# Performance work log

Measured on AMD Instinct MI355X. Metric: run time of the kernel, lower is better.

The kernel has to match this reference:

```python
import itertools
import jax, jax.numpy as jnp
import numpy as np
from jax import lax

INT_STEPS = 7
DOWN = 2


def _sample(vol, coords):
    """Trilinear sample vol [C, D, H, W] at voxel coords [3, D2, H2, W2].
    Matches torch grid_sample(align_corners=True, padding_mode='zeros') after
    voxelmorph's voxel->[-1,1] normalization (i.e. plain voxel coordinates)."""
    dims = vol.shape[1:]
    c0f = jnp.floor(coords)
    frac = coords - c0f
    c0 = c0f.astype(jnp.int32)
    out = jnp.zeros((vol.shape[0],) + coords.shape[1:], vol.dtype)
    for corner in itertools.product((0, 1), repeat=3):
        w = jnp.ones(coords.shape[1:], vol.dtype)
        valid = True
        idxs = []
        for ax in range(3):
            idx = c0[ax] + corner[ax]
            w = w * (frac[ax] if corner[ax] else 1.0 - frac[ax])
            valid = valid & (idx >= 0) & (idx < dims[ax])
            idxs.append(jnp.clip(idx, 0, dims[ax] - 1))
        out = out + vol[:, idxs[0], idxs[1], idxs[2]] * (w * valid)
    return out


def _grid(shape, dtype):
    return jnp.stack(jnp.meshgrid(*[jnp.arange(s, dtype=dtype) for s in shape], indexing='ij'))


def _warp(src, flow):
    # SpatialTransformer: sample src at identity grid + flow (voxel coords)
    return _sample(src, _grid(src.shape[1:], flow.dtype) + flow)


def _resize(x, out_shape):
    # F.interpolate trilinear, align_corners=True: src = i*(in-1)/(out-1)
    coords = jnp.stack(jnp.meshgrid(
        *[jnp.linspace(0.0, s_in - 1.0, s_out, dtype=x.dtype)
          for s_in, s_out in zip(x.shape[1:], out_shape)], indexing='ij'))
    return _sample(x, coords)


def _flow_single(pos_flow, label):
    # pos_flow: [3, D, H, W], label: [1, D, H, W]
    full = pos_flow.shape[1:]
    down_shape = tuple(s // DOWN for s in full)
    # ResizeTransform(int_downsize): factor=1/DOWN<1 -> resize then scale
    f = _resize(pos_flow, down_shape) * (1.0 / DOWN)
    # VecInt: scaling and squaring
    f = f * (1.0 / (2 ** INT_STEPS))
    for _ in range(INT_STEPS):
        f = f + _warp(f, f)
    # ResizeTransform(1/int_downsize): factor=DOWN>1 -> scale then resize
    f = _resize(f * float(DOWN), full)
    moved = _warp(label, f)
    return moved, f


def setup_inputs() -> dict:
    key = jax.random.key(0)
    k1, k2, k3 = jax.random.split(key, 3)
    B, F, D, H, W = 1, 16, 128, 128, 128
    features = jax.random.normal(k1, (B, F, D, H, W), jnp.float32)
    moving_label = jax.random.uniform(k2, (B, 1, D, H, W), jnp.float32)
    # conv weight initialized Normal(0, 1e-5), bias zeros (as in module)
    weight = jax.random.normal(k3, (3, F, 3, 3, 3), jnp.float32) * 1e-5
    bias = jnp.zeros((3,), jnp.float32)
    return {"features": features, "moving_label": moving_label,
            "weight": weight, "bias": bias}


def reference(features, moving_label, weight, bias):
    pos_flow = lax.conv_general_dilated(
        features, weight, window_strides=(1, 1, 1),
        padding=[(1, 1)] * 3,
        dimension_numbers=('NCDHW', 'OIDHW', 'NCDHW'))
    pos_flow = pos_flow + bias[None, :, None, None, None]
    moved, flow = jax.vmap(_flow_single)(pos_flow, moving_label)
    return moved, flow
```

## Files before the change

kernel.cpp:

```cpp
#include <hip/hip_runtime.h>
#include <hip/hip_bf16.h>


#define V128 2097152
#define V64  262144

template <int C>
__device__ __forceinline__ void trisample(const float* __restrict__ vol,
                                          int D, int H, int W, int cstride,
                                          float cz, float cy, float cx,
                                          float* out) {
    float fz = floorf(cz), fy = floorf(cy), fx = floorf(cx);
    int iz = (int)fz, iy = (int)fy, ix = (int)fx;
    float tz = cz - fz, ty = cy - fy, tx = cx - fx;
#pragma unroll
    for (int c = 0; c < C; ++c) out[c] = 0.0f;
#pragma unroll
    for (int dz = 0; dz < 2; ++dz) {
#pragma unroll
        for (int dy = 0; dy < 2; ++dy) {
#pragma unroll
            for (int dx = 0; dx < 2; ++dx) {
                int z = iz + dz, y = iy + dy, x = ix + dx;
                float w = (dz ? tz : 1.0f - tz) *
                          (dy ? ty : 1.0f - ty) *
                          (dx ? tx : 1.0f - tx);
                bool valid = (z >= 0) && (z < D) && (y >= 0) && (y < H) &&
                             (x >= 0) && (x < W);
                int zc = min(max(z, 0), D - 1);
                int yc = min(max(y, 0), H - 1);
                int xc = min(max(x, 0), W - 1);
                int base = (zc * H + yc) * W + xc;
                float wv = valid ? w : 0.0f;
#pragma unroll
                for (int c = 0; c < C; ++c)
                    out[c] += vol[c * cstride + base] * wv;
            }
        }
    }
}

template <int SI>
__device__ __forceinline__ void lds_lerp3(const float* __restrict__ f,
                                          float pz, float py, float px,
                                          float* out) {
    constexpr int NI = SI * SI * SI;
    float fz = floorf(pz), fy = floorf(py), fx = floorf(px);
    int iz = (int)fz, iy = (int)fy, ix = (int)fx;
    float tz = pz - fz, ty = py - fy, tx = px - fx;
    int b = (iz * SI + iy) * SI + ix;
    float wz0 = 1.0f - tz, wy0 = 1.0f - ty, wx0 = 1.0f - tx;
#pragma unroll
    for (int c = 0; c < 3; ++c) {
        const float* fc = f + c * NI;
        float v00 = fc[b] * wx0 + fc[b + 1] * tx;
        float v01 = fc[b + SI] * wx0 + fc[b + SI + 1] * tx;
        float v10 = fc[b + SI * SI] * wx0 + fc[b + SI * SI + 1] * tx;
        float v11 = fc[b + SI * SI + SI] * wx0 + fc[b + SI * SI + SI + 1] * tx;
        out[c] = wz0 * (wy0 * v00 + ty * v01) + tz * (wy0 * v10 + ty * v11);
    }
}

template <int SI>
__device__ __forceinline__ void step_lds(const float* __restrict__ in,
                                         float* __restrict__ out, int tid) {
    constexpr int SO = SI - 2;
    constexpr int NI = SI * SI * SI;
    constexpr int NO = SO * SO * SO;
    for (int i = tid; i < NO; i += 256) {
        int xx = i % SO, yy = (i / SO) % SO, zz = i / (SO * SO);
        int la = ((zz + 1) * SI + (yy + 1)) * SI + (xx + 1);
        float fz = in[la], fy = in[la + NI], fx = in[la + 2 * NI];
        float sm[3];
        lds_lerp3<SI>(in, (zz + 1) + fz, (yy + 1) + fy, (xx + 1) + fx, sm);
        out[i] = fz + sm[0];
        out[i + NO] = fy + sm[1];
        out[i + 2 * NO] = fx + sm[2];
    }
}

__device__ __forceinline__ void step_to_global(const float* __restrict__ in,
                                               float* __restrict__ gout,
                                               int tx, int ty, int tz,
                                               int tid) {
    constexpr int SI = 10;
    constexpr int NI = SI * SI * SI;
    for (int i = tid; i < 512; i += 256) {
        int xx = i & 7, yy = (i >> 3) & 7, zz = i >> 6;
        int la = ((zz + 1) * SI + (yy + 1)) * SI + (xx + 1);
        float fz = in[la], fy = in[la + NI], fx = in[la + 2 * NI];
        float sm[3];
        lds_lerp3<SI>(in, (zz + 1) + fz, (yy + 1) + fy, (xx + 1) + fx, sm);
        int n = ((tz + zz) << 12) + ((ty + yy) << 6) + (tx + xx);
        gout[n] = fz + sm[0];
        gout[n + V64] = fy + sm[1];
        gout[n + 2 * V64] = fx + sm[2];
    }
}

__global__ __launch_bounds__(256) void conv_kernel(
    const float* __restrict__ feat, const float* __restrict__ weight,
    const float* __restrict__ bias, float* __restrict__ pos_flow) {
    __shared__ float smem[2][3960];
    const int tid = threadIdx.x;
    const int x0 = blockIdx.x * 64, y0 = blockIdx.y * 4, z0 = blockIdx.z * 8;
    const int lx = tid & 63, ly = tid >> 6;

    int goff[16];
    unsigned vmask = 0;
    {
        int xx = tid % 66;
        int r = tid / 66;
        int yy = r % 6;
        int zz = r / 6;
#pragma unroll
        for (int k = 0; k < 16; ++k) {
            bool intile = (k < 15) || (tid < 120);
            int gx = x0 + xx - 1, gy = y0 + yy - 1, gz = z0 + zz - 1;
            bool ok = intile && ((unsigned)gx < 128u) &&
                      ((unsigned)gy < 128u) && ((unsigned)gz < 128u);
            goff[k] = (gz << 14) + (gy << 7) + gx;
            if (ok) vmask |= (1u << k);
            xx += 58;
            yy += 3;
            if (xx >= 66) { xx -= 66; yy += 1; }
            if (yy >= 6) { yy -= 6; zz += 1; }
        }
    }

    typedef __attribute__((ext_vector_type(2))) float f32x2;
    f32x2 acc[3][4];
#pragma unroll
    for (int o = 0; o < 3; ++o)
#pragma unroll
        for (int zp = 0; zp < 4; ++zp) acc[o][zp] = (f32x2)(0.0f);

    {
        float vals[16];
#pragma unroll
        for (int k = 0; k < 16; ++k) {
            vals[k] = 0.0f;
            if (vmask & (1u << k)) vals[k] = feat[goff[k]];
        }
#pragma unroll
        for (int k = 0; k < 16; ++k)
            if (k < 15 || tid < 120) smem[0][tid + 256 * k] = vals[k];
    }

    for (int c = 0; c < 16; ++c) {
        __syncthreads();
        if (c + 1 < 16) {
            const float* fc = feat + ((c + 1) << 21);
            float* buf = smem[(c + 1) & 1];
            float vals[16];
#pragma unroll
            for (int k = 0; k < 16; ++k) {
                vals[k] = 0.0f;
                if (vmask & (1u << k)) vals[k] = fc[goff[k]];
            }
#pragma unroll
            for (int k = 0; k < 16; ++k)
                if (k < 15 || tid < 120) buf[tid + 256 * k] = vals[k];
        }
        const float* buf = smem[c & 1];
        const float* wc = weight + c * 27;
#pragma unroll
        for (int dy = 0; dy < 3; ++dy) {
#pragma unroll
            for (int dx = 0; dx < 3; ++dx) {
                const float* p = buf + (ly + dy) * 66 + lx + dx;
                float v[10];
#pragma unroll
                for (int zz = 0; zz < 10; ++zz) v[zz] = p[zz * 396];
#pragma unroll
                for (int dz = 0; dz < 3; ++dz) {
#pragma unroll
                    for (int o = 0; o < 3; ++o) {
                        float w = wc[o * 432 + dz * 9 + dy * 3 + dx];
#pragma unroll
                        for (int zp = 0; zp < 4; ++zp) {
                            acc[o][zp].x += v[2 * zp + dz] * w;
                            acc[o][zp].y += v[2 * zp + dz + 1] * w;
                        }
                    }
                }
            }
        }
    }

#pragma unroll
    for (int o = 0; o < 3; ++o) {
        float b = bias[o];
#pragma unroll
        for (int zp = 0; zp < 4; ++zp) {
            int z = z0 + 2 * zp;
            int base = o * V128 + ((y0 + ly) << 7) + x0 + lx;
            pos_flow[base + (z << 14)] = acc[o][zp].x + b;
            pos_flow[base + ((z + 1) << 14)] = acc[o][zp].y + b;
        }
    }
}

__global__ __launch_bounds__(256) void f2_kernel(
    const float* __restrict__ pos_flow, float* __restrict__ gout) {
    __shared__ float A[3 * 2744];
    __shared__ float B[3 * 1728];
    const int tid = threadIdx.x;
    const int tx = blockIdx.x * 8, ty = blockIdx.y * 8, tz = blockIdx.z * 8;
    const int rbx = tx - 3, rby = ty - 3, rbz = tz - 3;
    const float s2 = 127.0f / 63.0f;
    const float k = 1.0f / 256.0f;
    for (int i = tid; i < 2744; i += 256) {
        int xx = i % 14, yy = (i / 14) % 14, zz = i / 196;
        int gz = rbz + zz, gy = rby + yy, gx = rbx + xx;
        float v[3] = {0.0f, 0.0f, 0.0f};
        if ((unsigned)gz < 64u && (unsigned)gy < 64u && (unsigned)gx < 64u)
            trisample<3>(pos_flow, 128, 128, 128, V128, gz * s2, gy * s2,
                         gx * s2, v);
        A[i] = v[0] * k;
        A[i + 2744] = v[1] * k;
        A[i + 2 * 2744] = v[2] * k;
    }
    __syncthreads();
    step_lds<14>(A, B, tid);
    __syncthreads();
    step_lds<12>(B, A, tid);
    __syncthreads();
    step_to_global(A, gout, tx, ty, tz, tid);
}

__global__ __launch_bounds__(256) void f3_kernel(
    const float* __restrict__ gin, float* __restrict__ gout) {
    __shared__ float A[3 * 2744];
    __shared__ float B[3 * 1728];
    const int tid = threadIdx.x;
    const int tx = blockIdx.x * 8, ty = blockIdx.y * 8, tz = blockIdx.z * 8;
    const int rbx = tx - 3, rby = ty - 3, rbz = tz - 3;
    for (int i = tid; i < 2744; i += 256) {
        int xx = i % 14, yy = (i / 14) % 14, zz = i / 196;
        int gz = rbz + zz, gy = rby + yy, gx = rbx + xx;
        float v0 = 0.0f, v1 = 0.0f, v2 = 0.0f;
        if ((unsigned)gz < 64u && (unsigned)gy < 64u && (unsigned)gx < 64u) {
            int n = (gz << 12) + (gy << 6) + gx;
            v0 = gin[n];
            v1 = gin[n + V64];
            v2 = gin[n + 2 * V64];
        }
        A[i] = v0;
        A[i + 2744] = v1;
        A[i + 2 * 2744] = v2;
    }
    __syncthreads();
    step_lds<14>(A, B, tid);
    __syncthreads();
    step_lds<12>(B, A, tid);
    __syncthreads();
    step_to_global(A, gout, tx, ty, tz, tid);
}

__global__ __launch_bounds__(256) void f4_kernel(
    const float* __restrict__ gin, const float* __restrict__ label,
    float* __restrict__ moved, float* __restrict__ flow) {
    __shared__ float A[3 * 2197];
    __shared__ float B[3 * 1331];
    const int tid = threadIdx.x;
    const int ttx = blockIdx.x, tty = blockIdx.y, ttz = blockIdx.z;
    const int r0x = (1008 * ttx) / 127 - 1;
    const int r0y = (1008 * tty) / 127 - 1;
    const int r0z = (1008 * ttz) / 127 - 1;
    const int rbx = r0x - 1, rby = r0y - 1, rbz = r0z - 1;
    for (int i = tid; i < 2197; i += 256) {
        int xx = i % 13, yy = (i / 13) % 13, zz = i / 169;
        int gz = rbz + zz, gy = rby + yy, gx = rbx + xx;
        float v0 = 0.0f, v1 = 0.0f, v2 = 0.0f;
        if ((unsigned)gz < 64u && (unsigned)gy < 64u && (unsigned)gx < 64u) {
            int n = (gz << 12) + (gy << 6) + gx;
            v0 = gin[n];
            v1 = gin[n + V64];
            v2 = gin[n + 2 * V64];
        }
        A[i] = v0;
        A[i + 2197] = v1;
        A[i + 2 * 2197] = v2;
    }
    __syncthreads();
    step_lds<13>(A, B, tid);
    __syncthreads();
    const float s3 = 63.0f / 127.0f;
    for (int i = tid; i < 4096; i += 256) {
        int lx = i & 15, ly = (i >> 4) & 15, lz = i >> 8;
        int gx = ttx * 16 + lx, gy = tty * 16 + ly, gz = ttz * 16 + lz;
        float f[3];
        lds_lerp3<11>(B, gz * s3 - (float)r0z, gy * s3 - (float)r0y,
                      gx * s3 - (float)r0x, f);
        float fz = 2.0f * f[0], fy = 2.0f * f[1], fx = 2.0f * f[2];
        int m = (gz << 14) + (gy << 7) + gx;
        flow[m] = fz;
        flow[m + V128] = fy;
        flow[m + 2 * V128] = fx;
        float mv[1];
        trisample<1>(label, 128, 128, 128, 0, gz + fz, gy + fy, gx + fx, mv);
        moved[m] = mv[0];
    }
}

extern "C" void kernel_launch(void* const* d_in, const int* in_sizes, int n_in,
                              void* d_out, int out_size, void* d_ws,
                              size_t ws_size, hipStream_t stream) {
    const float* features = (const float*)d_in[0];
    const float* label = (const float*)d_in[1];
    const float* weight = (const float*)d_in[2];
    const float* bias = (const float*)d_in[3];
    float* out = (float*)d_out;
    float* moved = out;
    float* flow = out + V128;
    float* fA = (float*)d_ws;
    float* fB = fA + 3 * V64;

    conv_kernel<<<dim3(2, 32, 16), 256, 0, stream>>>(features, weight, bias,
                                                     flow);
    f2_kernel<<<dim3(8, 8, 8), 256, 0, stream>>>(flow, fA);
    f3_kernel<<<dim3(8, 8, 8), 256, 0, stream>>>(fA, fB);
    f4_kernel<<<dim3(8, 8, 8), 256, 0, stream>>>(fB, label, moved, flow);
}
```

Before: 327.7 us.

## Fuse four kernels into one persistent kernel with grid-wide barriers

Merges the conv, two squaring-step kernels and the final resize/warp kernel into one persistent kernel of 512 blocks, separated by a software grid barrier built on atomics in workspace memory. Each block runs two conv tiles, then one tile of each later stage. This removes three kernel launch boundaries and their tail gaps. In exchange it relies on all 512 blocks being co-resident (launch bounds of 2 blocks per CU) and adds barrier spin cost, and the conv stage now runs with fewer blocks in flight.

After: 635.5 us. +93.9%, slower.

```diff
diff --git a/kernel.cpp b/kernel.cpp
--- a/kernel.cpp
+++ b/kernel.cpp
@@ -1,9 +1,33 @@
 #include <hip/hip_runtime.h>
-#include <hip/hip_bf16.h>
 
 
 #define V128 2097152
 #define V64  262144
+#define NBLK 512
+
+__device__ __forceinline__ void gbar(unsigned* bar) {
+    __syncthreads();
+    if (threadIdx.x == 0) {
+        __threadfence();
+        unsigned g = __hip_atomic_load(bar + 1, __ATOMIC_RELAXED,
+                                       __HIP_MEMORY_SCOPE_AGENT);
+        unsigned prev = __hip_atomic_fetch_add(bar, 1u, __ATOMIC_ACQ_REL,
+                                               __HIP_MEMORY_SCOPE_AGENT);
+        if (prev == NBLK - 1) {
+            __hip_atomic_store(bar, 0u, __ATOMIC_RELAXED,
+                               __HIP_MEMORY_SCOPE_AGENT);
+            __hip_atomic_fetch_add(bar + 1, 1u, __ATOMIC_ACQ_REL,
+                                   __HIP_MEMORY_SCOPE_AGENT);
+        } else {
+            while (__hip_atomic_load(bar + 1, __ATOMIC_ACQUIRE,
+                                     __HIP_MEMORY_SCOPE_AGENT) == g) {
+                __builtin_amdgcn_s_sleep(8);
+            }
+        }
+        __threadfence();
+    }
+    __syncthreads();
+}
 
 template <int C>
 __device__ __forceinline__ void trisample(const float* __restrict__ vol,
@@ -98,12 +122,13 @@
     }
 }
 
-__global__ __launch_bounds__(256) void conv_kernel(
-    const float* __restrict__ feat, const float* __restrict__ weight,
-    const float* __restrict__ bias, float* __restrict__ pos_flow) {
-    __shared__ float smem[2][3960];
+__device__ void conv_tile(const float* __restrict__ feat,
+                          const float* __restrict__ weight,
+                          const float* __restrict__ bias,
+                          float* __restrict__ pos_flow,
+                          float* __restrict__ sm, int x0, int y0, int z0) {
+    float (*smem)[3960] = (float (*)[3960])sm;
     const int tid = threadIdx.x;
-    const int x0 = blockIdx.x * 64, y0 = blockIdx.y * 4, z0 = blockIdx.z * 8;
     const int lx = tid & 63, ly = tid >> 6;
 
     int goff[16];
@@ -201,12 +226,12 @@
     }
 }
 
-__global__ __launch_bounds__(256) void f2_kernel(
-    const float* __restrict__ pos_flow, float* __restrict__ gout) {
-    __shared__ float A[3 * 2744];
-    __shared__ float B[3 * 1728];
+__device__ void f2_body(const float* __restrict__ pos_flow,
+                        float* __restrict__ gout, float* __restrict__ sm,
+                        int tx, int ty, int tz) {
+    float* A = sm;
+    float* B = sm + 3 * 2744;
     const int tid = threadIdx.x;
-    const int tx = blockIdx.x * 8, ty = blockIdx.y * 8, tz = blockIdx.z * 8;
     const int rbx = tx - 3, rby = ty - 3, rbz = tz - 3;
     const float s2 = 127.0f / 63.0f;
     const float k = 1.0f / 256.0f;
@@ -229,12 +254,12 @@
     step_to_global(A, gout, tx, ty, tz, tid);
 }
 
-__global__ __launch_bounds__(256) void f3_kernel(
-    const float* __restrict__ gin, float* __restrict__ gout) {
-    __shared__ float A[3 * 2744];
-    __shared__ float B[3 * 1728];
+__device__ void f3_body(const float* __restrict__ gin,
+                        float* __restrict__ gout, float* __restrict__ sm,
+                        int tx, int ty, int tz) {
+    float* A = sm;
+    float* B = sm + 3 * 2744;
     const int tid = threadIdx.x;
-    const int tx = blockIdx.x * 8, ty = blockIdx.y * 8, tz = blockIdx.z * 8;
     const int rbx = tx - 3, rby = ty - 3, rbz = tz - 3;
     for (int i = tid; i < 2744; i += 256) {
         int xx = i % 14, yy = (i / 14) % 14, zz = i / 196;
@@ -258,13 +283,13 @@
     step_to_global(A, gout, tx, ty, tz, tid);
 }
 
-__global__ __launch_bounds__(256) void f4_kernel(
-    const float* __restrict__ gin, const float* __restrict__ label,
-    float* __restrict__ moved, float* __restrict__ flow) {
-    __shared__ float A[3 * 2197];
-    __shared__ float B[3 * 1331];
+__device__ void f4_body(const float* __restrict__ gin,
+                        const float* __restrict__ label,
+                        float* __restrict__ moved, float* __restrict__ flow,
+                        float* __restrict__ sm, int ttx, int tty, int ttz) {
+    float* A = sm;
+    float* B = sm + 3 * 2197;
     const int tid = threadIdx.x;
-    const int ttx = blockIdx.x, tty = blockIdx.y, ttz = blockIdx.z;
     const int r0x = (1008 * ttx) / 127 - 1;
     const int r0y = (1008 * tty) / 127 - 1;
     const int r0z = (1008 * ttz) / 127 - 1;
@@ -304,6 +329,33 @@
     }
 }
 
+__global__ __launch_bounds__(256, 2) void mega_kernel(
+    const float* __restrict__ feat, const float* __restrict__ weight,
+    const float* __restrict__ bias, const float* __restrict__ label,
+    float* __restrict__ moved, float* __restrict__ flow,
+    float* __restrict__ fA, float* __restrict__ fB, unsigned* bar) {
+    __shared__ float sm[13416];
+    const int bid = blockIdx.x;
+
+    for (int job = bid; job < 1024; job += NBLK) {
+        int x0 = (job & 1) * 64;
+        int y0 = ((job >> 1) & 31) * 4;
+        int z0 = (job >> 6) * 8;
+        conv_tile(feat, weight, bias, flow, sm, x0, y0, z0);
+        __syncthreads();
+    }
+    gbar(bar);
+
+    f2_body(flow, fA, sm, (bid & 7) * 8, ((bid >> 3) & 7) * 8,
+            (bid >> 6) * 8);
+    gbar(bar);
+
+    f3_body(fA, fB, sm, (bid & 7) * 8, ((bid >> 3) & 7) * 8, (bid >> 6) * 8);
+    gbar(bar);
+
+    f4_body(fB, label, moved, flow, sm, bid & 7, (bid >> 3) & 7, bid >> 6);
+}
+
 extern "C" void kernel_launch(void* const* d_in, const int* in_sizes, int n_in,
                               void* d_out, int out_size, void* d_ws,
                               size_t ws_size, hipStream_t stream) {
@@ -316,10 +368,10 @@
     float* flow = out + V128;
     float* fA = (float*)d_ws;
     float* fB = fA + 3 * V64;
-
-    conv_kernel<<<dim3(2, 32, 16), 256, 0, stream>>>(features, weight, bias,
-                                                     flow);
-    f2_kernel<<<dim3(8, 8, 8), 256, 0, stream>>>(flow, fA);
-    f3_kernel<<<dim3(8, 8, 8), 256, 0, stream>>>(fA, fB);
-    f4_kernel<<<dim3(8, 8, 8), 256, 0, stream>>>(fB, label, moved, flow);
-}
+    size_t bar_off = (ws_size - 64) & ~(size_t)63;
+    unsigned* bar = (unsigned*)((char*)d_ws + bar_off);
+
+    hipMemsetAsync(bar, 0, 16, stream);
+    mega_kernel<<<dim3(NBLK), dim3(256), 0, stream>>>(
+        features, weight, bias, label, moved, flow, fA, fB, bar);
+}
```

## Interleave flow channels and store conv LDS tile z-innermost for vector reads

Applied to the files above, without the earlier changes.

Intermediate flow buffers (conv output, the low-res integration steps) switch from channel-planar to interleaved xyz-per-voxel layout, so each trilinear corner fetch touches one contiguous 12-byte group instead of three distant planes. The conv shared tile is re-laid out with z innermost, so the per-thread z column is read as aligned and unaligned float2 vector loads, and accumulation uses packed float2 FMAs. f2 resampling gets an inlined sampler with clamped indices that skips the per-corner validity checks. The interleaved stride-3 stores are less coalesced, and z-innermost LDS reads with stride 10 may cause bank conflicts.

Measured after the change: 331.5 us. Within noise of the previous version (+1.2%).

```diff
diff --git a/kernel.cpp b/kernel.cpp
--- a/kernel.cpp
+++ b/kernel.cpp
@@ -1,9 +1,11 @@
 #include <hip/hip_runtime.h>
-#include <hip/hip_bf16.h>
 
 
 #define V128 2097152
 #define V64  262144
+
+typedef __attribute__((ext_vector_type(2))) float f32x2;
+typedef float f32x2u __attribute__((ext_vector_type(2), aligned(4)));
 
 template <int C>
 __device__ __forceinline__ void trisample(const float* __restrict__ vol,
@@ -91,16 +93,16 @@
         float fz = in[la], fy = in[la + NI], fx = in[la + 2 * NI];
         float sm[3];
         lds_lerp3<SI>(in, (zz + 1) + fz, (yy + 1) + fy, (xx + 1) + fx, sm);
-        int n = ((tz + zz) << 12) + ((ty + yy) << 6) + (tx + xx);
-        gout[n] = fz + sm[0];
-        gout[n + V64] = fy + sm[1];
-        gout[n + 2 * V64] = fx + sm[2];
+        int n3 = ((((tz + zz) << 12) + ((ty + yy) << 6) + (tx + xx))) * 3;
+        gout[n3] = fz + sm[0];
+        gout[n3 + 1] = fy + sm[1];
+        gout[n3 + 2] = fx + sm[2];
     }
 }
 
 __global__ __launch_bounds__(256) void conv_kernel(
     const float* __restrict__ feat, const float* __restrict__ weight,
-    const float* __restrict__ bias, float* __restrict__ pos_flow) {
+    const float* __restrict__ bias, float* __restrict__ pf) {
     __shared__ float smem[2][3960];
     const int tid = threadIdx.x;
     const int x0 = blockIdx.x * 64, y0 = blockIdx.y * 4, z0 = blockIdx.z * 8;
@@ -108,27 +110,21 @@
 
     int goff[16];
     unsigned vmask = 0;
-    {
-        int xx = tid % 66;
-        int r = tid / 66;
-        int yy = r % 6;
-        int zz = r / 6;
-#pragma unroll
-        for (int k = 0; k < 16; ++k) {
-            bool intile = (k < 15) || (tid < 120);
-            int gx = x0 + xx - 1, gy = y0 + yy - 1, gz = z0 + zz - 1;
-            bool ok = intile && ((unsigned)gx < 128u) &&
-                      ((unsigned)gy < 128u) && ((unsigned)gz < 128u);
-            goff[k] = (gz << 14) + (gy << 7) + gx;
-            if (ok) vmask |= (1u << k);
-            xx += 58;
-            yy += 3;
-            if (xx >= 66) { xx -= 66; yy += 1; }
-            if (yy >= 6) { yy -= 6; zz += 1; }
-        }
-    }
-
-    typedef __attribute__((ext_vector_type(2))) float f32x2;
+#pragma unroll
+    for (int k = 0; k < 16; ++k) {
+        int s = tid + 256 * k;
+        int zz = s % 10;
+        int r = s / 10;
+        int xx = r % 66;
+        int yy = r / 66;
+        bool intile = (k < 15) || (tid < 120);
+        int gx = x0 + xx - 1, gy = y0 + yy - 1, gz = z0 + zz - 1;
+        bool ok = intile && ((unsigned)gx < 128u) && ((unsigned)gy < 128u) &&
+                  ((unsigned)gz < 128u);
+        goff[k] = (gz << 14) + (gy << 7) + gx;
+        if (ok) vmask |= (1u << k);
+    }
+
     f32x2 acc[3][4];
 #pragma unroll
     for (int o = 0; o < 3; ++o)
@@ -168,41 +164,47 @@
         for (int dy = 0; dy < 3; ++dy) {
 #pragma unroll
             for (int dx = 0; dx < 3; ++dx) {
-                const float* p = buf + (ly + dy) * 66 + lx + dx;
-                float v[10];
-#pragma unroll
-                for (int zz = 0; zz < 10; ++zz) v[zz] = p[zz * 396];
-#pragma unroll
-                for (int dz = 0; dz < 3; ++dz) {
-#pragma unroll
-                    for (int o = 0; o < 3; ++o) {
-                        float w = wc[o * 432 + dz * 9 + dy * 3 + dx];
-#pragma unroll
-                        for (int zp = 0; zp < 4; ++zp) {
-                            acc[o][zp].x += v[2 * zp + dz] * w;
-                            acc[o][zp].y += v[2 * zp + dz + 1] * w;
-                        }
+                const float* p = buf + ((ly + dy) * 66 + lx + dx) * 10;
+                f32x2 pv[5];
+                f32x2 qv[4];
+#pragma unroll
+                for (int k2 = 0; k2 < 5; ++k2)
+                    pv[k2] = *(const f32x2*)(p + 2 * k2);
+#pragma unroll
+                for (int k2 = 0; k2 < 4; ++k2)
+                    qv[k2] = *(const f32x2u*)(p + 2 * k2 + 1);
+#pragma unroll
+                for (int o = 0; o < 3; ++o) {
+                    float w0 = wc[o * 432 + 0 + dy * 3 + dx];
+                    float w1 = wc[o * 432 + 9 + dy * 3 + dx];
+                    float w2 = wc[o * 432 + 18 + dy * 3 + dx];
+#pragma unroll
+                    for (int zp = 0; zp < 4; ++zp) {
+                        acc[o][zp] += pv[zp] * (f32x2)(w0);
+                        acc[o][zp] += qv[zp] * (f32x2)(w1);
+                        acc[o][zp] += pv[zp + 1] * (f32x2)(w2);
                     }
                 }
             }
         }
     }
 
-#pragma unroll
-    for (int o = 0; o < 3; ++o) {
-        float b = bias[o];
-#pragma unroll
-        for (int zp = 0; zp < 4; ++zp) {
-            int z = z0 + 2 * zp;
-            int base = o * V128 + ((y0 + ly) << 7) + x0 + lx;
-            pos_flow[base + (z << 14)] = acc[o][zp].x + b;
-            pos_flow[base + ((z + 1) << 14)] = acc[o][zp].y + b;
+    float b0 = bias[0], b1 = bias[1], b2 = bias[2];
+#pragma unroll
+    for (int zp = 0; zp < 4; ++zp) {
+        int vox0 = ((z0 + 2 * zp) << 14) + ((y0 + ly) << 7) + x0 + lx;
+#pragma unroll
+        for (int h = 0; h < 2; ++h) {
+            int m3 = (vox0 + (h << 14)) * 3;
+            pf[m3] = (h ? acc[0][zp].y : acc[0][zp].x) + b0;
+            pf[m3 + 1] = (h ? acc[1][zp].y : acc[1][zp].x) + b1;
+            pf[m3 + 2] = (h ? acc[2][zp].y : acc[2][zp].x) + b2;
         }
     }
 }
 
 __global__ __launch_bounds__(256) void f2_kernel(
-    const float* __restrict__ pos_flow, float* __restrict__ gout) {
+    const float* __restrict__ pf, float* __restrict__ gout) {
     __shared__ float A[3 * 2744];
     __shared__ float B[3 * 1728];
     const int tid = threadIdx.x;
@@ -213,13 +215,35 @@
     for (int i = tid; i < 2744; i += 256) {
         int xx = i % 14, yy = (i / 14) % 14, zz = i / 196;
         int gz = rbz + zz, gy = rby + yy, gx = rbx + xx;
-        float v[3] = {0.0f, 0.0f, 0.0f};
-        if ((unsigned)gz < 64u && (unsigned)gy < 64u && (unsigned)gx < 64u)
-            trisample<3>(pos_flow, 128, 128, 128, V128, gz * s2, gy * s2,
-                         gx * s2, v);
-        A[i] = v[0] * k;
-        A[i + 2744] = v[1] * k;
-        A[i + 2 * 2744] = v[2] * k;
+        float v0 = 0.0f, v1 = 0.0f, v2 = 0.0f;
+        if ((unsigned)gz < 64u && (unsigned)gy < 64u && (unsigned)gx < 64u) {
+            float cz = gz * s2, cy = gy * s2, cx = gx * s2;
+            int iz = min((int)cz, 126);
+            int iy = min((int)cy, 126);
+            int ix = min((int)cx, 126);
+            float tzf = cz - (float)iz;
+            float tyf = cy - (float)iy;
+            float txf = cx - (float)ix;
+            float wz[2] = {1.0f - tzf, tzf};
+            float wy[2] = {1.0f - tyf, tyf};
+            float wx[2] = {1.0f - txf, txf};
+            int b = ((iz << 14) + (iy << 7) + ix) * 3;
+#pragma unroll
+            for (int dz = 0; dz < 2; ++dz)
+#pragma unroll
+                for (int dy = 0; dy < 2; ++dy)
+#pragma unroll
+                    for (int dx = 0; dx < 2; ++dx) {
+                        float w = wz[dz] * wy[dy] * wx[dx];
+                        int bb = b + dz * (3 << 14) + dy * (3 << 7) + dx * 3;
+                        v0 += pf[bb] * w;
+                        v1 += pf[bb + 1] * w;
+                        v2 += pf[bb + 2] * w;
+                    }
+        }
+        A[i] = v0 * k;
+        A[i + 2744] = v1 * k;
+        A[i + 2 * 2744] = v2 * k;
     }
     __syncthreads();
     step_lds<14>(A, B, tid);
@@ -241,10 +265,10 @@
         int gz = rbz + zz, gy = rby + yy, gx = rbx + xx;
         float v0 = 0.0f, v1 = 0.0f, v2 = 0.0f;
         if ((unsigned)gz < 64u && (unsigned)gy < 64u && (unsigned)gx < 64u) {
-            int n = (gz << 12) + (gy << 6) + gx;
-            v0 = gin[n];
-            v1 = gin[n + V64];
-            v2 = gin[n + 2 * V64];
+            int n3 = ((gz << 12) + (gy << 6) + gx) * 3;
+            v0 = gin[n3];
+            v1 = gin[n3 + 1];
+            v2 = gin[n3 + 2];
         }
         A[i] = v0;
         A[i + 2744] = v1;
@@ -274,10 +298,10 @@
         int gz = rbz + zz, gy = rby + yy, gx = rbx + xx;
         float v0 = 0.0f, v1 = 0.0f, v2 = 0.0f;
         if ((unsigned)gz < 64u && (unsigned)gy < 64u && (unsigned)gx < 64u) {
-            int n = (gz << 12) + (gy << 6) + gx;
-            v0 = gin[n];
-            v1 = gin[n + V64];
-            v2 = gin[n + 2 * V64];
+            int n3 = ((gz << 12) + (gy << 6) + gx) * 3;
+            v0 = gin[n3];
+            v1 = gin[n3 + 1];
+            v2 = gin[n3 + 2];
         }
         A[i] = v0;
         A[i + 2197] = v1;
```
